# Optimization experiments

Hardware: AMD Instinct MI355X
Metric: run time of the kernel (lower is better)

The kernel has to match this reference:

```python
import jax, jax.numpy as jnp
import numpy as np

N = 100000
E = 3200000
HID = 256
C = 10
T = 12
D = 8
HEADS = 4
LH = HID // 2  # LSTM hidden = hidden_dim // 2


def setup_inputs() -> dict:
    key = jax.random.key(0)
    ks = jax.random.split(key, 16)
    rn = lambda k, shp, s=0.05: jax.random.normal(k, shp, dtype=jnp.float32) * s
    return {
        "embeddings": jax.random.normal(ks[0], (N, HID), dtype=jnp.float32),
        "predictions": jax.random.normal(ks[1], (N, C), dtype=jnp.float32),
        "temporal_features": jax.random.normal(ks[2], (N, T, D), dtype=jnp.float32),
        "edge_index": jax.random.randint(ks[3], (2, E), 0, N),
        "cW1": rn(ks[4], (HID // 2, HID)), "cb1": jnp.zeros((HID // 2,), jnp.float32),
        "cW2": rn(ks[5], (1, HID // 2)), "cb2": jnp.zeros((1,), jnp.float32),
        "w_ih0": rn(ks[6], (4 * LH, C)), "w_hh0": rn(ks[7], (4 * LH, LH)),
        "b_ih0": jnp.zeros((4 * LH,), jnp.float32), "b_hh0": jnp.zeros((4 * LH,), jnp.float32),
        "w_ih1": rn(ks[8], (4 * LH, LH)), "w_hh1": rn(ks[9], (4 * LH, LH)),
        "b_ih1": jnp.zeros((4 * LH,), jnp.float32), "b_hh1": jnp.zeros((4 * LH,), jnp.float32),
        "gW": rn(ks[10], (C, HEADS * C)), "ga_src": rn(ks[11], (HEADS, C)),
        "ga_dst": rn(ks[12], (HEADS, C)), "gb": jnp.zeros((C,), jnp.float32),
    }


def _lstm_layer(x, w_ih, w_hh, b_ih, b_hh):
    # x: [N, T, I]; PyTorch gate order i, f, g, o
    n = x.shape[0]
    h_dim = w_hh.shape[1]
    def step(carry, xt):
        h, c = carry
        g = xt @ w_ih.T + h @ w_hh.T + b_ih + b_hh  # [N, 4H]
        i, f, gg, o = jnp.split(g, 4, axis=-1)
        c = jax.nn.sigmoid(f) * c + jax.nn.sigmoid(i) * jnp.tanh(gg)
        h = jax.nn.sigmoid(o) * jnp.tanh(c)
        return (h, c), h
    init = (jnp.zeros((n, h_dim), x.dtype), jnp.zeros((n, h_dim), x.dtype))
    _, hs = jax.lax.scan(step, init, jnp.swapaxes(x, 0, 1))  # [T, N, H]
    return jnp.swapaxes(hs, 0, 1)


def _gat(probs, src, dst, gW, ga_src, ga_dst, gb, n):
    x = (probs @ gW).reshape(n, HEADS, C)  # [N, H, C]
    a_s = (x * ga_src).sum(-1)  # [N, H]
    a_d = (x * ga_dst).sum(-1)
    e = jax.nn.leaky_relu(a_s[src] + a_d[dst], 0.2)  # [E, H]
    m = jax.ops.segment_max(e, dst, num_segments=n)
    ex = jnp.exp(e - m[dst])
    s = jax.ops.segment_sum(ex, dst, num_segments=n)
    alpha = ex / (s[dst] + 1e-16)  # edge softmax per destination
    out = jax.ops.segment_sum(alpha[:, :, None] * x[src], dst, num_segments=n)
    return out.mean(axis=1) + gb  # concat=False -> head mean, plus bias


def reference(embeddings, predictions, temporal_features, edge_index,
              cW1, cb1, cW2, cb2,
              w_ih0, w_hh0, b_ih0, b_hh0, w_ih1, w_hh1, b_ih1, b_hh1,
              gW, ga_src, ga_dst, gb):
    n = predictions.shape[0]
    probs = jax.nn.softmax(predictions, axis=-1)
    max_probs = probs.max(axis=-1)
    pseudo_labels = jnp.argmax(probs, axis=-1)

    # confidence_net (dropout inactive in eval)
    h = jax.nn.relu(embeddings @ cW1.T + cb1)
    embedding_confidence = jax.nn.sigmoid(h @ cW2.T + cb2)[:, 0]

    # temporal consistency: same prediction repeated T times through 2-layer LSTM
    t = temporal_features.shape[1]
    pred_seq = jnp.broadcast_to(predictions[:, None, :], (n, t, predictions.shape[1]))
    l1 = _lstm_layer(pred_seq, w_ih0, w_hh0, b_ih0, b_hh0)
    l2 = _lstm_layer(l1, w_ih1, w_hh1, b_ih1, b_hh1)
    temporal_variance = jnp.var(l2, axis=1, ddof=1).mean(axis=-1)  # torch.var unbiased
    temporal_confidence = 1.0 / (1.0 + temporal_variance)

    # self-loops (used by both GATConv and agreement check)
    loops = jnp.arange(n, dtype=edge_index.dtype)
    src = jnp.concatenate([edge_index[0], loops])
    dst = jnp.concatenate([edge_index[1], loops])

    gout = _gat(probs, src, dst, gW, ga_src, ga_dst, gb, n)
    num = (probs * gout).sum(-1)
    den = jnp.maximum(jnp.linalg.norm(probs, axis=-1) * jnp.linalg.norm(gout, axis=-1), 1e-8)
    graph_confidence = ((num / den) + 1.0) / 2.0

    combined = (0.4 * max_probs + 0.2 * embedding_confidence
                + 0.2 * temporal_confidence + 0.2 * graph_confidence)
    confident_mask = combined > 0.85

    # neighborhood agreement via segment-sum scatter (replaces per-edge loop)
    deg = jax.ops.segment_sum(jnp.ones_like(src, jnp.float32), src, num_segments=n)
    oh = jax.nn.one_hot(pseudo_labels, C, dtype=jnp.float32)
    nsum = jax.ops.segment_sum(oh[src], dst, num_segments=n)
    navg = nsum / (deg[:, None] + 1e-8)
    agreement = jnp.take_along_axis(navg, pseudo_labels[:, None], axis=1)[:, 0] >= 0.6
    final_mask = confident_mask & agreement

    entropy = -(probs * jnp.log(probs + 1e-8)).sum(-1)
    uncertainty = entropy / np.log(C).astype(np.float32)

    return (pseudo_labels, combined, final_mask, max_probs,
            embedding_confidence, temporal_confidence, graph_confidence, uncertainty)
```

## Files before the change

kernel.cpp:

```cpp
#include <hip/hip_runtime.h>
#include <hip/hip_bf16.h>


#define HIDN 256
#define NC 10
#define TSTEPS 12
#define NHEADS 4
#define LH 128

typedef __attribute__((ext_vector_type(8))) short short8;
typedef __attribute__((ext_vector_type(4))) float floatx4;

__device__ __forceinline__ unsigned short f2bf(float x) {
  unsigned u = __float_as_uint(x);
  u = u + 0x7FFFu + ((u >> 16) & 1u);
  return (unsigned short)(u >> 16);
}
__device__ __forceinline__ unsigned char f2fp8(float x) {
  return (unsigned char)(__builtin_amdgcn_cvt_pk_fp8_f32(x, 0.f, 0, false) & 0xff);
}
__device__ __forceinline__ float fexp2(float x) { return __builtin_amdgcn_exp2f(x); }
__device__ __forceinline__ float frcpf(float x) { return __builtin_amdgcn_rcpf(x); }
#define LOG2E 1.44269504f
__device__ __forceinline__ float sigf(float x) {
  return frcpf(1.0f + fexp2(-LOG2E * x));
}
__device__ __forceinline__ float sig2(float x) {
  return frcpf(1.f + fexp2(-LOG2E * x));
}
__device__ __forceinline__ float tanh2(float x) {
  return 1.f - 2.f * frcpf(1.f + fexp2((2.f * LOG2E) * x));
}
__device__ __forceinline__ floatx4 mfma16(short8 a, short8 b, floatx4 c) {
  return __builtin_amdgcn_mfma_f32_16x16x32_bf16(a, b, c, 0, 0, 0);
}
__device__ __forceinline__ floatx4 mfma8(long a, long b, floatx4 c) {
  return __builtin_amdgcn_mfma_f32_16x16x32_fp8_fp8(a, b, c, 0, 0, 0);
}

__global__ __launch_bounds__(256) void probs_kernel(
    const float* __restrict__ pred, const float* __restrict__ gW,
    const float* __restrict__ gas, const float* __restrict__ gad,
    float* __restrict__ out, float* __restrict__ wp12,
    float* __restrict__ was, float* __restrict__ wad,
    int* __restrict__ wlab, float* __restrict__ wmp, int N) {
  __shared__ float sgW[400], sgas[40], sgad[40];
  int tid = threadIdx.x;
  for (int i = tid; i < 400; i += 256) sgW[i] = gW[i];
  if (tid < 40) { sgas[tid] = gas[tid]; sgad[tid] = gad[tid]; }
  __syncthreads();
  int node = blockIdx.x * 256 + tid;
  if (node >= N) return;
  const float* pr = pred + (size_t)node * NC;
  float p[NC];
#pragma unroll
  for (int c = 0; c < NC; c++) p[c] = pr[c];
  float pm = p[0]; int arg = 0;
#pragma unroll
  for (int c = 1; c < NC; c++) if (p[c] > pm) { pm = p[c]; arg = c; }
  float s = 0.f, prb[NC];
#pragma unroll
  for (int c = 0; c < NC; c++) { prb[c] = __expf(p[c] - pm); s += prb[c]; }
  float inv = 1.f / s;
  float ent = 0.f;
#pragma unroll
  for (int c = 0; c < NC; c++) {
    prb[c] *= inv;
    ent -= prb[c] * __logf(prb[c] + 1e-8f);
  }
  float4* wp = (float4*)(wp12 + (size_t)node * 12);
  wp[0] = make_float4(prb[0], prb[1], prb[2], prb[3]);
  wp[1] = make_float4(prb[4], prb[5], prb[6], prb[7]);
  wp[2] = make_float4(prb[8], prb[9], 0.f, 0.f);
  out[node] = (float)arg;
  out[(size_t)3 * N + node] = inv;
  out[(size_t)7 * N + node] = ent * (1.f / 2.302585093f);
  wlab[node] = arg;
  wmp[node] = inv;
  float xv[40];
#pragma unroll
  for (int hc = 0; hc < 40; hc++) {
    float t = 0.f;
#pragma unroll
    for (int k = 0; k < NC; k++) t += prb[k] * sgW[k * 40 + hc];
    xv[hc] = t;
  }
#pragma unroll
  for (int h = 0; h < NHEADS; h++) {
    float as = 0.f, ad = 0.f;
#pragma unroll
    for (int c = 0; c < NC; c++) { as += xv[h * 10 + c] * sgas[h * 10 + c]; ad += xv[h * 10 + c] * sgad[h * 10 + c]; }
    was[(size_t)node * 4 + h] = as;
    wad[(size_t)node * 4 + h] = ad;
  }
}

__global__ __launch_bounds__(256) void pack_kernel(
    const float* __restrict__ whh0, const float* __restrict__ wih0,
    const float* __restrict__ wih1, const float* __restrict__ whh1,
    const float* __restrict__ cw1,
    unsigned char* __restrict__ PB1, unsigned char* __restrict__ PB2,
    unsigned short* __restrict__ PBc) {
  int idx = blockIdx.x * 256 + threadIdx.x;
  if (idx < 81920) {
    int j = idx & 7, lane = (idx >> 3) & 63, rest = idx >> 9;
    int g = rest & 3, w = (rest >> 2) & 7, ks = rest >> 5;
    int k = ks * 32 + ((lane >> 4) << 3) + j;
    int u = w * 16 + (lane & 15), row = g * 128 + u;
    float val = 0.f;
    if (k < 128) val = whh0[row * 128 + k];
    else if (k < 138) val = wih0[row * 10 + (k - 128)];
    PB1[idx] = f2fp8(val);
  }
  if (idx < 131072) {
    int j = idx & 7, lane = (idx >> 3) & 63, rest = idx >> 9;
    int g = rest & 3, w = (rest >> 2) & 7, ks = rest >> 5;
    int k = ks * 32 + ((lane >> 4) << 3) + j;
    int u = w * 16 + (lane & 15), row = g * 128 + u;
    float val = (k < 128) ? wih1[row * 128 + k] : whh1[row * 128 + (k - 128)];
    PB2[idx] = f2fp8(val);
  }
  if (idx < 32768) {
    int j = idx & 7, lane = (idx >> 3) & 63, t2 = idx >> 9;
    int ti = t2 & 7, ks = t2 >> 3;
    int n = ti * 16 + (lane & 15);
    int k = ks * 32 + ((lane >> 4) << 3) + j;
    PBc[idx] = f2bf(cw1[n * 256 + k]);
  }
}

__global__ void rankhist_kernel(const int* __restrict__ ei, int* __restrict__ indeg,
                                int* __restrict__ outdeg, int* __restrict__ erank,
                                int E, int N) {
  int idx = blockIdx.x * 256 + threadIdx.x;
  if (idx >= E + N) return;
  int src, dst;
  if (idx < E) { src = ei[idx]; dst = ei[E + idx]; } else { src = dst = idx - E; }
  int r = atomicAdd(&indeg[dst], 1);
  atomicAdd(&outdeg[src], 1);
  erank[idx] = r;
}

__device__ __forceinline__ void conf_body(
    int bb, unsigned short* astage,
    const float* __restrict__ emb, const unsigned short* __restrict__ PBc,
    const float* __restrict__ cb1, const float* __restrict__ cw2,
    const float* __restrict__ cb2, float* __restrict__ wec, int N) {
  int tid = threadIdx.x;
  int base = bb * 128;
  for (int i = tid * 4; i < 128 * 256; i += 1024) {
    int row = i >> 8, col = i & 255;
    float4 v = make_float4(0.f, 0.f, 0.f, 0.f);
    if (base + row < N) v = *(const float4*)(emb + (size_t)(base + row) * 256 + col);
    unsigned short* d = &astage[row * 264 + col];
    d[0] = f2bf(v.x); d[1] = f2bf(v.y); d[2] = f2bf(v.z); d[3] = f2bf(v.w);
  }
  __syncthreads();
  int wave = tid >> 6, lane = tid & 63, quad = lane >> 4, ln = lane & 15;
  float b1f[8], w2f[8];
#pragma unroll
  for (int t = 0; t < 8; t++) { b1f[t] = cb1[t * 16 + ln]; w2f[t] = cw2[t * 16 + ln]; }
  floatx4 acc[2][8];
#pragma unroll
  for (int mi = 0; mi < 2; mi++)
#pragma unroll
    for (int t = 0; t < 8; t++) acc[mi][t] = (floatx4){b1f[t], b1f[t], b1f[t], b1f[t]};
#pragma unroll
  for (int ks = 0; ks < 8; ks++) {
    short8 a0 = *(const short8*)&astage[(wave * 32 + ln) * 264 + ks * 32 + quad * 8];
    short8 a1 = *(const short8*)&astage[(wave * 32 + 16 + ln) * 264 + ks * 32 + quad * 8];
    const unsigned short* bp = PBc + (((size_t)(ks * 8) * 64 + lane) << 3);
#pragma unroll
    for (int t = 0; t < 8; t++) {
      short8 b = *(const short8*)(bp + (size_t)t * 512);
      acc[0][t] = mfma16(a0, b, acc[0][t]);
      acc[1][t] = mfma16(a1, b, acc[1][t]);
    }
  }
  float part[2][4];
#pragma unroll
  for (int mi = 0; mi < 2; mi++)
#pragma unroll
    for (int r = 0; r < 4; r++) {
      float t = 0.f;
#pragma unroll
      for (int ti = 0; ti < 8; ti++) t += fmaxf(acc[mi][ti][r], 0.f) * w2f[ti];
      part[mi][r] = t;
    }
#pragma unroll
  for (int off = 8; off >= 1; off >>= 1)
#pragma unroll
    for (int mi = 0; mi < 2; mi++)
#pragma unroll
      for (int r = 0; r < 4; r++) part[mi][r] += __shfl_xor(part[mi][r], off);
  if (ln == 0) {
    float b2 = cb2[0];
#pragma unroll
    for (int mi = 0; mi < 2; mi++)
#pragma unroll
      for (int r = 0; r < 4; r++) {
        int node = base + wave * 32 + mi * 16 + quad * 4 + r;
        if (node < N) wec[node] = sigf(part[mi][r] + b2);
      }
  }
}

__device__ __forceinline__ void scan_body(
    int* wsum, const int* __restrict__ indeg, int* __restrict__ rowptr, int N) {
  int t = threadIdx.x;
  int lane = t & 63, wv = t >> 6;
  int runbase = 0;
  for (int c0 = 0; c0 < N; c0 += 1024) {
    int i = c0 + t * 4;
    int v0 = 0, v1 = 0, v2 = 0, v3 = 0;
    if (i + 0 < N) v0 = indeg[i + 0];
    if (i + 1 < N) v1 = indeg[i + 1];
    if (i + 2 < N) v2 = indeg[i + 2];
    if (i + 3 < N) v3 = indeg[i + 3];
    int tsum = v0 + v1 + v2 + v3;
    int x = tsum;
#pragma unroll
    for (int d = 1; d < 64; d <<= 1) { int y = __shfl_up(x, d); if (lane >= d) x += y; }
    if (lane == 63) wsum[wv] = x;
    __syncthreads();
    int wo = 0;
    for (int w = 0; w < wv; w++) wo += wsum[w];
    int tot = wsum[0] + wsum[1] + wsum[2] + wsum[3];
    int excl = runbase + wo + x - tsum;
    if (i + 0 < N) rowptr[i + 0] = excl;
    if (i + 1 < N) rowptr[i + 1] = excl + v0;
    if (i + 2 < N) rowptr[i + 2] = excl + v0 + v1;
    if (i + 3 < N) rowptr[i + 3] = excl + v0 + v1 + v2;
    runbase += tot;
    __syncthreads();
  }
  if (t == 0) rowptr[N] = runbase;
}

__global__ __launch_bounds__(256) void mega2_kernel(
    const float* __restrict__ emb, const unsigned short* __restrict__ PBc,
    const float* __restrict__ cb1, const float* __restrict__ cw2,
    const float* __restrict__ cb2, float* __restrict__ wec,
    const int* __restrict__ indeg, int* __restrict__ rowptr, int N, int GC) {
  __shared__ __align__(16) unsigned short astage[128 * 264];
  int b = blockIdx.x;
  if (b < GC) {
    conf_body(b, astage, emb, PBc, cb1, cw2, cb2, wec, N);
  } else {
    scan_body((int*)astage, indeg, rowptr, N);
  }
}

__global__ void scatterrank_kernel(const int* __restrict__ ei,
                                   const int* __restrict__ rowptr,
                                   const int* __restrict__ erank,
                                   int* __restrict__ csr, int E, int N) {
  int idx = blockIdx.x * 256 + threadIdx.x;
  if (idx >= E + N) return;
  int src, dst;
  if (idx < E) { src = ei[idx]; dst = ei[E + idx]; } else { src = dst = idx - E; }
  csr[rowptr[dst] + erank[idx]] = src;
}

__global__ __launch_bounds__(256) void gather_kernel(
    const int* __restrict__ rowptr, const int* __restrict__ csr,
    const float* __restrict__ was, const float* __restrict__ wad,
    const float* __restrict__ wp12, const int* __restrict__ wlab,
    const int* __restrict__ outdeg, const float* __restrict__ gW,
    const float* __restrict__ gb, float* __restrict__ wgc,
    float* __restrict__ wag, int N) {
  __shared__ float sgW[400];
  int tid = threadIdx.x;
  for (int i = tid; i < 400; i += 256) sgW[i] = gW[i];
  __syncthreads();
  int vgid = blockIdx.x * 256 + tid;
  int node = vgid >> 4, sub = vgid & 15, h = sub & 3, par = sub >> 2;
  if (node >= N) return;
  int beg = rowptr[node], end = rowptr[node + 1];
  float ad = wad[(size_t)node * 4 + h];
  int mylab = wlab[node];
  float ssum = 0.f, cnt = 0.f;
  float z[10];
#pragma unroll
  for (int c = 0; c < 10; c++) z[c] = 0.f;
  for (int e = beg + par; e < end; e += 4) {
    int s = csr[e];
    float v = was[(size_t)s * 4 + h] + ad;
    float lr = v >= 0.f ? v : 0.2f * v;
    float ex = fexp2(LOG2E * lr);
    ssum += ex;
    const float4* pp = (const float4*)(wp12 + (size_t)s * 12);
    float4 p0 = pp[0], p1 = pp[1], p2 = pp[2];
    z[0] += ex * p0.x; z[1] += ex * p0.y; z[2] += ex * p0.z; z[3] += ex * p0.w;
    z[4] += ex * p1.x; z[5] += ex * p1.y; z[6] += ex * p1.z; z[7] += ex * p1.w;
    z[8] += ex * p2.x; z[9] += ex * p2.y;
    cnt += (wlab[s] == mylab) ? 1.f : 0.f;
  }
  ssum += __shfl_xor(ssum, 4); ssum += __shfl_xor(ssum, 8);
  cnt  += __shfl_xor(cnt, 4);  cnt  += __shfl_xor(cnt, 8);
#pragma unroll
  for (int c = 0; c < 10; c++) { z[c] += __shfl_xor(z[c], 4); z[c] += __shfl_xor(z[c], 8); }
  float inv = 1.f / (ssum + 1e-16f);
  float gpart[10];
#pragma unroll
  for (int c = 0; c < 10; c++) {
    float t = 0.f;
#pragma unroll
    for (int k = 0; k < 10; k++) t += z[k] * sgW[k * 40 + h * 10 + c];
    gpart[c] = t * inv;
  }
#pragma unroll
  for (int c = 0; c < 10; c++) {
    gpart[c] += __shfl_xor(gpart[c], 1);
    gpart[c] += __shfl_xor(gpart[c], 2);
  }
  if (sub == 0) {
    float num = 0.f, np2 = 0.f, ng2 = 0.f;
    const float* pn = wp12 + (size_t)node * 12;
#pragma unroll
    for (int c = 0; c < 10; c++) {
      float g = gpart[c] * 0.25f + gb[c];
      float p = pn[c];
      num += p * g;
      np2 += p * p;
      ng2 += g * g;
    }
    float den = fmaxf(sqrtf(np2) * sqrtf(ng2), 1e-8f);
    wgc[node] = (num / den + 1.f) * 0.5f;
    float dgv = (float)outdeg[node];
    wag[node] = cnt / (dgv + 1e-8f);
  }
}

#define HB2 4352

__global__ __launch_bounds__(512, 2) void lstm_kernel(
    const float* __restrict__ pred, const unsigned char* __restrict__ PB1,
    const unsigned char* __restrict__ PB2,
    const float* __restrict__ bih0, const float* __restrict__ bhh0,
    const float* __restrict__ bih1, const float* __restrict__ bhh1,
    const float* __restrict__ wmp, const float* __restrict__ wec,
    const float* __restrict__ wgc, const float* __restrict__ wag,
    float* __restrict__ out, int N) {
  __shared__ __align__(16) unsigned char hb[4 * HB2];
  __shared__ __align__(16) unsigned char xbuf[32 * 40];
  __shared__ float varsum[32];
  int tid = threadIdx.x;
  int base = blockIdx.x * 32;
  for (int i = tid * 4; i < HB2; i += 2048) *(int*)&hb[3 * HB2 + i] = 0;
  for (int i = tid; i < 32 * 40; i += 512) {
    int nd = i / 40, o = i - nd * 40;
    float v = 0.f;
    if (o < 10 && base + nd < N) v = pred[(size_t)(base + nd) * NC + o];
    xbuf[i] = f2fp8(v);
  }
  if (tid < 32) varsum[tid] = 0.f;
  int wave = tid >> 6, lane = tid & 63, quad = lane >> 4, ln = lane & 15;
  float b0f[4], b1f[4];
#pragma unroll
  for (int g = 0; g < 4; g++) {
    int row = g * 128 + wave * 16 + ln;
    b0f[g] = bih0[row] + bhh0[row];
    b1f[g] = bih1[row] + bhh1[row];
  }
  long w1r[5][4], w2r[8][4];
#pragma unroll
  for (int ks = 0; ks < 5; ks++)
#pragma unroll
    for (int g = 0; g < 4; g++)
      w1r[ks][g] = *(const long*)(PB1 + (size_t)(((ks * 8 + wave) * 4 + g) * 64 + lane) * 8);
#pragma unroll
  for (int ks = 0; ks < 8; ks++)
#pragma unroll
    for (int g = 0; g < 4; g++)
      w2r[ks][g] = *(const long*)(PB2 + (size_t)(((ks * 8 + wave) * 4 + g) * 64 + lane) * 8);
  float c1[8], c2[8], s1[8], s2[8];
#pragma unroll
  for (int i = 0; i < 8; i++) { c1[i] = 0.f; c2[i] = 0.f; s1[i] = 0.f; s2[i] = 0.f; }
  const int hq = quad * 8;
  const int ucol = wave * 16 + ln;
  int arow[2], wrow[2];
#pragma unroll
  for (int mt = 0; mt < 2; mt++) {
    arow[mt] = (mt * 16 + ln) * 136 + hq;
    wrow[mt] = (mt * 16 + quad * 4) * 136 + ucol;
  }
  __syncthreads();
  long xa[2];
  xa[0] = *(const long*)&xbuf[ln * 40 + hq];
  xa[1] = *(const long*)&xbuf[(16 + ln) * 40 + hq];

  {
    floatx4 acc[2][4];
#pragma unroll
    for (int mt = 0; mt < 2; mt++)
#pragma unroll
      for (int g = 0; g < 4; g++) acc[mt][g] = (floatx4){b0f[g], b0f[g], b0f[g], b0f[g]};
#pragma unroll
    for (int g = 0; g < 4; g++)
#pragma unroll
      for (int mt = 0; mt < 2; mt++) acc[mt][g] = mfma8(xa[mt], w1r[4][g], acc[mt][g]);
#pragma unroll
    for (int mt = 0; mt < 2; mt++)
#pragma unroll
      for (int r = 0; r < 4; r++) {
        int ci = mt * 4 + r;
        float ig = sig2(acc[mt][0][r]);
        float gg = tanh2(acc[mt][2][r]);
        float og = sig2(acc[mt][3][r]);
        float c = ig * gg;
        c1[ci] = c;
        hb[0 + wrow[mt] + r * 136] = f2fp8(og * tanh2(c));
      }
  }

#define LSTM_SEG(O1R, O1W, O2R, O2W, lastseg)                                    \
  {                                                                              \
    __syncthreads();                                                             \
    floatx4 acc[2][4];                                                           \
    _Pragma("unroll") for (int mt = 0; mt < 2; mt++)                             \
        _Pragma("unroll") for (int g = 0; g < 4; g++)                            \
            acc[mt][g] = (floatx4){b1f[g], b1f[g], b1f[g], b1f[g]};              \
    _Pragma("unroll") for (int ks = 0; ks < 8; ks++) {                           \
      long a_[2];                                                                \
      if (ks < 4) {                                                              \
        _Pragma("unroll") for (int mt = 0; mt < 2; mt++)                         \
            a_[mt] = *(const long*)&hb[(O1R) + arow[mt] + ks * 32];              \
      } else {                                                                   \
        _Pragma("unroll") for (int mt = 0; mt < 2; mt++)                         \
            a_[mt] = *(const long*)&hb[(O2R) + arow[mt] + (ks - 4) * 32];        \
      }                                                                          \
      _Pragma("unroll") for (int g = 0; g < 4; g++)                              \
          _Pragma("unroll") for (int mt = 0; mt < 2; mt++)                       \
              acc[mt][g] = mfma8(a_[mt], w2r[ks][g], acc[mt][g]);                \
    }                                                                            \
    _Pragma("unroll") for (int mt = 0; mt < 2; mt++)                             \
        _Pragma("unroll") for (int r = 0; r < 4; r++) {                          \
      int ci = mt * 4 + r;                                                       \
      float ig = sig2(acc[mt][0][r]);                                            \
      float fg = sig2(acc[mt][1][r]);                                            \
      float gg = tanh2(acc[mt][2][r]);                                           \
      float og = sig2(acc[mt][3][r]);                                            \
      float c = fg * c2[ci] + ig * gg;                                           \
      c2[ci] = c;                                                                \
      float h = og * tanh2(c);                                                   \
      s1[ci] += h;                                                               \
      s2[ci] += h * h;                                                           \
      hb[(O2W) + wrow[mt] + r * 136] = f2fp8(h);                                 \
    }                                                                            \
    if (!(lastseg)) {                                                            \
      _Pragma("unroll") for (int mt = 0; mt < 2; mt++)                           \
          _Pragma("unroll") for (int g = 0; g < 4; g++)                          \
              acc[mt][g] = (floatx4){b0f[g], b0f[g], b0f[g], b0f[g]};            \
      _Pragma("unroll") for (int ks = 0; ks < 5; ks++) {                         \
        long a_[2];                                                              \
        if (ks < 4) {                                                            \
          _Pragma("unroll") for (int mt = 0; mt < 2; mt++)                       \
              a_[mt] = *(const long*)&hb[(O1R) + arow[mt] + ks * 32];            \
        } else {                                                                 \
          a_[0] = xa[0]; a_[1] = xa[1];                                          \
        }                                                                        \
        _Pragma("unroll") for (int g = 0; g < 4; g++)                            \
            _Pragma("unroll") for (int mt = 0; mt < 2; mt++)                     \
                acc[mt][g] = mfma8(a_[mt], w1r[ks][g], acc[mt][g]);              \
      }                                                                          \
      _Pragma("unroll") for (int mt = 0; mt < 2; mt++)                           \
          _Pragma("unroll") for (int r = 0; r < 4; r++) {                        \
        int ci = mt * 4 + r;                                                     \
        float ig = sig2(acc[mt][0][r]);                                          \
        float fg = sig2(acc[mt][1][r]);                                          \
        float gg = tanh2(acc[mt][2][r]);                                         \
        float og = sig2(acc[mt][3][r]);                                          \
        float c = fg * c1[ci] + ig * gg;                                         \
        c1[ci] = c;                                                              \
        hb[(O1W) + wrow[mt] + r * 136] = f2fp8(og * tanh2(c));                   \
      }                                                                          \
    }                                                                            \
  }

  for (int tt = 0; tt < TSTEPS / 2; tt++) {
    LSTM_SEG(0, HB2, 3 * HB2, 2 * HB2, false);
    LSTM_SEG(HB2, 0, 2 * HB2, 3 * HB2, tt == TSTEPS / 2 - 1);
  }
#undef LSTM_SEG

#pragma unroll
  for (int mt = 0; mt < 2; mt++)
#pragma unroll
    for (int r = 0; r < 4; r++) {
      int ci = mt * 4 + r;
      float m = s1[ci] * (1.f / 12.f);
      float var = (s2[ci] - 12.f * m * m) * (1.f / 11.f);
      atomicAdd(&varsum[mt * 16 + quad * 4 + r], var);
    }
  __syncthreads();
  if (tid < 32 && base + tid < N) {
    int node = base + tid;
    float tc = 1.f / (1.f + varsum[tid] * (1.f / 128.f));
    float mp = wmp[node], ec = wec[node], gc = wgc[node];
    float comb = 0.4f * mp + 0.2f * ec + 0.2f * tc + 0.2f * gc;
    bool mask = (comb > 0.85f) && (wag[node] >= 0.6f);
    out[(size_t)1 * N + node] = comb;
    out[(size_t)2 * N + node] = mask ? 1.f : 0.f;
    out[(size_t)4 * N + node] = ec;
    out[(size_t)5 * N + node] = tc;
    out[(size_t)6 * N + node] = gc;
  }
}

extern "C" void kernel_launch(void* const* d_in, const int* in_sizes, int n_in,
                              void* d_out, int out_size, void* d_ws, size_t ws_size,
                              hipStream_t stream) {
  const float* emb  = (const float*)d_in[0];
  const float* pred = (const float*)d_in[1];
  const int*   ei   = (const int*)d_in[3];
  const float* cw1  = (const float*)d_in[4];
  const float* cb1  = (const float*)d_in[5];
  const float* cw2  = (const float*)d_in[6];
  const float* cb2  = (const float*)d_in[7];
  const float* wih0 = (const float*)d_in[8];
  const float* whh0 = (const float*)d_in[9];
  const float* bih0 = (const float*)d_in[10];
  const float* bhh0 = (const float*)d_in[11];
  const float* wih1 = (const float*)d_in[12];
  const float* whh1 = (const float*)d_in[13];
  const float* bih1 = (const float*)d_in[14];
  const float* bhh1 = (const float*)d_in[15];
  const float* gW   = (const float*)d_in[16];
  const float* gas  = (const float*)d_in[17];
  const float* gad  = (const float*)d_in[18];
  const float* gb   = (const float*)d_in[19];

  const int N = in_sizes[0] / HIDN;
  const int E = in_sizes[3] / 2;
  float* out = (float*)d_out;
  float* ws = (float*)d_ws;
  const size_t sN = (size_t)N;
  const size_t sE = (size_t)E;

  float* wp12   = ws;
  float* was    = ws + 12 * sN;
  float* wad    = ws + 16 * sN;
  int*   wlab   = (int*)(ws + 20 * sN);
  float* wmp    = ws + 21 * sN;
  float* wec    = ws + 22 * sN;
  float* wgc    = ws + 24 * sN;
  float* wag    = ws + 25 * sN;
  int* indeg    = (int*)(ws + 26 * sN);
  int* outdeg   = (int*)(ws + 27 * sN);
  int* rowptr   = (int*)(ws + 28 * sN);
  int* erank    = (int*)(ws + 29 * sN) + 64;
  int* csr      = erank + sE + sN + 64;
  float* pbase  = (float*)(csr + sE + sN + 64);
  unsigned char* PB1 = (unsigned char*)pbase;
  unsigned char* PB2 = (unsigned char*)(pbase + 20480);
  unsigned short* PBc = (unsigned short*)(pbase + 53248);

  hipMemsetAsync(indeg, 0, 2 * sN * sizeof(int), stream);

  probs_kernel<<<(N + 255) / 256, 256, 0, stream>>>(
      pred, gW, gas, gad, out, wp12, was, wad, wlab, wmp, N);
  pack_kernel<<<512, 256, 0, stream>>>(whh0, wih0, wih1, whh1, cw1, PB1, PB2, PBc);
  int ne = E + N;
  rankhist_kernel<<<(ne + 255) / 256, 256, 0, stream>>>(ei, indeg, outdeg, erank, E, N);

  int GC = (N + 127) / 128;
  mega2_kernel<<<GC + 1, 256, 0, stream>>>(
      emb, PBc, cb1, cw2, cb2, wec, indeg, rowptr, N, GC);

  scatterrank_kernel<<<(ne + 255) / 256, 256, 0, stream>>>(ei, rowptr, erank, csr, E, N);

  gather_kernel<<<(16 * N + 255) / 256, 256, 0, stream>>>(
      rowptr, csr, was, wad, wp12, wlab, outdeg, gW, gb, wgc, wag, N);

  lstm_kernel<<<(N + 31) / 32, 512, 0, stream>>>(
      pred, PB1, PB2, bih0, bhh0, bih1, bhh1, wmp, wec, wgc, wag, out, N);
}
```

Before: 1.412 ms.

## Shard degree atomics, parallelize CSR scan, pack node records, and restructure GAT gather

Degree counting now goes into 8 sharded histograms keyed by block, which is meant to reduce atomic contention on hot nodes. The single-block serial prefix scan is replaced by a three-kernel parallel scan that also computes per-shard bases. Probabilities, source attention scores and the label are packed into one 64-byte record per node, so each edge needs a single contiguous fetch. The gather kernel uses 4 threads per node that process all heads per edge instead of 16 threads each handling one head, which cuts redundant neighbor loads but raises register use and adds extra kernel launches and memset traffic.

```diff
diff --git a/kernel.cpp b/kernel.cpp
--- a/kernel.cpp
+++ b/kernel.cpp
@@ -41,9 +41,8 @@
 __global__ __launch_bounds__(256) void probs_kernel(
     const float* __restrict__ pred, const float* __restrict__ gW,
     const float* __restrict__ gas, const float* __restrict__ gad,
-    float* __restrict__ out, float* __restrict__ wp12,
-    float* __restrict__ was, float* __restrict__ wad,
-    int* __restrict__ wlab, float* __restrict__ wmp, int N) {
+    float* __restrict__ out, float* __restrict__ wp16,
+    float* __restrict__ wad, float* __restrict__ wmp, int N) {
   __shared__ float sgW[400], sgas[40], sgad[40];
   int tid = threadIdx.x;
   for (int i = tid; i < 400; i += 256) sgW[i] = gW[i];
@@ -68,14 +67,9 @@
     prb[c] *= inv;
     ent -= prb[c] * __logf(prb[c] + 1e-8f);
   }
-  float4* wp = (float4*)(wp12 + (size_t)node * 12);
-  wp[0] = make_float4(prb[0], prb[1], prb[2], prb[3]);
-  wp[1] = make_float4(prb[4], prb[5], prb[6], prb[7]);
-  wp[2] = make_float4(prb[8], prb[9], 0.f, 0.f);
   out[node] = (float)arg;
   out[(size_t)3 * N + node] = inv;
   out[(size_t)7 * N + node] = ent * (1.f / 2.302585093f);
-  wlab[node] = arg;
   wmp[node] = inv;
   float xv[40];
 #pragma unroll
@@ -85,14 +79,20 @@
     for (int k = 0; k < NC; k++) t += prb[k] * sgW[k * 40 + hc];
     xv[hc] = t;
   }
+  float asv[4];
 #pragma unroll
   for (int h = 0; h < NHEADS; h++) {
     float as = 0.f, ad = 0.f;
 #pragma unroll
     for (int c = 0; c < NC; c++) { as += xv[h * 10 + c] * sgas[h * 10 + c]; ad += xv[h * 10 + c] * sgad[h * 10 + c]; }
-    was[(size_t)node * 4 + h] = as;
+    asv[h] = as;
     wad[(size_t)node * 4 + h] = ad;
   }
+  float4* wp = (float4*)(wp16 + (size_t)node * 16);
+  wp[0] = make_float4(prb[0], prb[1], prb[2], prb[3]);
+  wp[1] = make_float4(prb[4], prb[5], prb[6], prb[7]);
+  wp[2] = make_float4(prb[8], prb[9], asv[0], asv[1]);
+  wp[3] = make_float4(asv[2], asv[3], __int_as_float(arg), 0.f);
 }
 
 __global__ __launch_bounds__(256) void pack_kernel(
@@ -129,25 +129,26 @@
   }
 }
 
-__global__ void rankhist_kernel(const int* __restrict__ ei, int* __restrict__ indeg,
-                                int* __restrict__ outdeg, int* __restrict__ erank,
+__global__ void rankhist_kernel(const int* __restrict__ ei, int* __restrict__ shin,
+                                int* __restrict__ shout, int* __restrict__ erank,
                                 int E, int N) {
   int idx = blockIdx.x * 256 + threadIdx.x;
   if (idx >= E + N) return;
+  int sh = blockIdx.x & 7;
   int src, dst;
   if (idx < E) { src = ei[idx]; dst = ei[E + idx]; } else { src = dst = idx - E; }
-  int r = atomicAdd(&indeg[dst], 1);
-  atomicAdd(&outdeg[src], 1);
+  int r = atomicAdd(&shin[(size_t)sh * N + dst], 1);
+  atomicAdd(&shout[(size_t)sh * N + src], 1);
   erank[idx] = r;
 }
 
-__device__ __forceinline__ void conf_body(
-    int bb, unsigned short* astage,
+__global__ __launch_bounds__(256) void conf_kernel(
     const float* __restrict__ emb, const unsigned short* __restrict__ PBc,
     const float* __restrict__ cb1, const float* __restrict__ cw2,
     const float* __restrict__ cb2, float* __restrict__ wec, int N) {
+  __shared__ __align__(16) unsigned short astage[128 * 264];
   int tid = threadIdx.x;
-  int base = bb * 128;
+  int base = blockIdx.x * 128;
   for (int i = tid * 4; i < 128 * 256; i += 1024) {
     int row = i >> 8, col = i & 255;
     float4 v = make_float4(0.f, 0.f, 0.f, 0.f);
@@ -205,67 +206,90 @@
   }
 }
 
-__device__ __forceinline__ void scan_body(
-    int* wsum, const int* __restrict__ indeg, int* __restrict__ rowptr, int N) {
+__global__ __launch_bounds__(256) void scan1_kernel(
+    const int* __restrict__ shin, const int* __restrict__ shout,
+    int* __restrict__ shbase, int* __restrict__ outdeg,
+    int* __restrict__ rowptr, int* __restrict__ partials, int N) {
+  int t = threadIdx.x, b = blockIdx.x;
+  int base = b * 1024 + t * 4;
+  int tot[4];
+#pragma unroll
+  for (int j = 0; j < 4; j++) {
+    int i = base + j;
+    int run = 0;
+    if (i < N) {
+      int od = 0;
+#pragma unroll
+      for (int sh = 0; sh < 8; sh++) {
+        int v = shin[(size_t)sh * N + i];
+        shbase[(size_t)sh * N + i] = run;
+        run += v;
+        od += shout[(size_t)sh * N + i];
+      }
+      outdeg[i] = od;
+    }
+    tot[j] = run;
+  }
+  int tsum = tot[0] + tot[1] + tot[2] + tot[3];
+  int lane = t & 63, wv = t >> 6;
+  int x = tsum;
+#pragma unroll
+  for (int d = 1; d < 64; d <<= 1) { int y = __shfl_up(x, d); if (lane >= d) x += y; }
+  __shared__ int wsum[4];
+  if (lane == 63) wsum[wv] = x;
+  __syncthreads();
+  int wo = 0;
+  for (int i = 0; i < wv; i++) wo += wsum[i];
+  int excl = wo + x - tsum;
+  if (base + 0 < N) rowptr[base + 0] = excl;
+  if (base + 1 < N) rowptr[base + 1] = excl + tot[0];
+  if (base + 2 < N) rowptr[base + 2] = excl + tot[0] + tot[1];
+  if (base + 3 < N) rowptr[base + 3] = excl + tot[0] + tot[1] + tot[2];
+  if (t == 255) partials[b] = wo + x;
+}
+
+__global__ void scan2_kernel(int* __restrict__ partials, int nb) {
   int t = threadIdx.x;
   int lane = t & 63, wv = t >> 6;
-  int runbase = 0;
-  for (int c0 = 0; c0 < N; c0 += 1024) {
-    int i = c0 + t * 4;
-    int v0 = 0, v1 = 0, v2 = 0, v3 = 0;
-    if (i + 0 < N) v0 = indeg[i + 0];
-    if (i + 1 < N) v1 = indeg[i + 1];
-    if (i + 2 < N) v2 = indeg[i + 2];
-    if (i + 3 < N) v3 = indeg[i + 3];
-    int tsum = v0 + v1 + v2 + v3;
-    int x = tsum;
-#pragma unroll
-    for (int d = 1; d < 64; d <<= 1) { int y = __shfl_up(x, d); if (lane >= d) x += y; }
-    if (lane == 63) wsum[wv] = x;
-    __syncthreads();
-    int wo = 0;
-    for (int w = 0; w < wv; w++) wo += wsum[w];
-    int tot = wsum[0] + wsum[1] + wsum[2] + wsum[3];
-    int excl = runbase + wo + x - tsum;
-    if (i + 0 < N) rowptr[i + 0] = excl;
-    if (i + 1 < N) rowptr[i + 1] = excl + v0;
-    if (i + 2 < N) rowptr[i + 2] = excl + v0 + v1;
-    if (i + 3 < N) rowptr[i + 3] = excl + v0 + v1 + v2;
-    runbase += tot;
-    __syncthreads();
-  }
-  if (t == 0) rowptr[N] = runbase;
-}
-
-__global__ __launch_bounds__(256) void mega2_kernel(
-    const float* __restrict__ emb, const unsigned short* __restrict__ PBc,
-    const float* __restrict__ cb1, const float* __restrict__ cw2,
-    const float* __restrict__ cb2, float* __restrict__ wec,
-    const int* __restrict__ indeg, int* __restrict__ rowptr, int N, int GC) {
-  __shared__ __align__(16) unsigned short astage[128 * 264];
-  int b = blockIdx.x;
-  if (b < GC) {
-    conf_body(b, astage, emb, PBc, cb1, cw2, cb2, wec, N);
-  } else {
-    scan_body((int*)astage, indeg, rowptr, N);
-  }
+  int v = (t < nb) ? partials[t] : 0;
+  int x = v;
+#pragma unroll
+  for (int d = 1; d < 64; d <<= 1) { int y = __shfl_up(x, d); if (lane >= d) x += y; }
+  __shared__ int wsum[4];
+  if (lane == 63) wsum[wv] = x;
+  __syncthreads();
+  int wo = 0;
+  for (int i = 0; i < wv; i++) wo += wsum[i];
+  if (t < nb) partials[t] = wo + x - v;
+}
+
+__global__ void scan3_kernel(int* __restrict__ rowptr, int* __restrict__ shbase,
+                             const int* __restrict__ partials, int N, int total) {
+  int i = blockIdx.x * 256 + threadIdx.x;
+  if (i < N) {
+    int r = rowptr[i] + partials[i >> 10];
+    rowptr[i] = r;
+#pragma unroll
+    for (int sh = 0; sh < 8; sh++) shbase[(size_t)sh * N + i] += r;
+  }
+  if (i == 0) rowptr[N] = total;
 }
 
 __global__ void scatterrank_kernel(const int* __restrict__ ei,
-                                   const int* __restrict__ rowptr,
+                                   const int* __restrict__ shbase,
                                    const int* __restrict__ erank,
                                    int* __restrict__ csr, int E, int N) {
   int idx = blockIdx.x * 256 + threadIdx.x;
   if (idx >= E + N) return;
+  int sh = (idx >> 8) & 7;
   int src, dst;
   if (idx < E) { src = ei[idx]; dst = ei[E + idx]; } else { src = dst = idx - E; }
-  csr[rowptr[dst] + erank[idx]] = src;
+  csr[shbase[(size_t)sh * N + dst] + erank[idx]] = src;
 }
 
 __global__ __launch_bounds__(256) void gather_kernel(
     const int* __restrict__ rowptr, const int* __restrict__ csr,
-    const float* __restrict__ was, const float* __restrict__ wad,
-    const float* __restrict__ wp12, const int* __restrict__ wlab,
+    const float* __restrict__ wp16, const float* __restrict__ wad,
     const int* __restrict__ outdeg, const float* __restrict__ gW,
     const float* __restrict__ gb, float* __restrict__ wgc,
     float* __restrict__ wag, int N) {
@@ -274,39 +298,69 @@
   for (int i = tid; i < 400; i += 256) sgW[i] = gW[i];
   __syncthreads();
   int vgid = blockIdx.x * 256 + tid;
-  int node = vgid >> 4, sub = vgid & 15, h = sub & 3, par = sub >> 2;
+  int node = vgid >> 2, par = vgid & 3;
   if (node >= N) return;
   int beg = rowptr[node], end = rowptr[node + 1];
-  float ad = wad[(size_t)node * 4 + h];
-  int mylab = wlab[node];
-  float ssum = 0.f, cnt = 0.f;
-  float z[10];
-#pragma unroll
-  for (int c = 0; c < 10; c++) z[c] = 0.f;
+  float4 ad4 = *(const float4*)(wad + (size_t)node * 4);
+  const float4* myrec = (const float4*)(wp16 + (size_t)node * 16);
+  float4 m3 = myrec[3];
+  int mylab = __float_as_int(m3.z);
+  float ssum0 = 0.f, ssum1 = 0.f, ssum2 = 0.f, ssum3 = 0.f, cnt = 0.f;
+  float z[4][10];
+#pragma unroll
+  for (int h = 0; h < 4; h++)
+#pragma unroll
+    for (int c = 0; c < 10; c++) z[h][c] = 0.f;
   for (int e = beg + par; e < end; e += 4) {
     int s = csr[e];
-    float v = was[(size_t)s * 4 + h] + ad;
-    float lr = v >= 0.f ? v : 0.2f * v;
-    float ex = fexp2(LOG2E * lr);
-    ssum += ex;
-    const float4* pp = (const float4*)(wp12 + (size_t)s * 12);
-    float4 p0 = pp[0], p1 = pp[1], p2 = pp[2];
-    z[0] += ex * p0.x; z[1] += ex * p0.y; z[2] += ex * p0.z; z[3] += ex * p0.w;
-    z[4] += ex * p1.x; z[5] += ex * p1.y; z[6] += ex * p1.z; z[7] += ex * p1.w;
-    z[8] += ex * p2.x; z[9] += ex * p2.y;
-    cnt += (wlab[s] == mylab) ? 1.f : 0.f;
-  }
-  ssum += __shfl_xor(ssum, 4); ssum += __shfl_xor(ssum, 8);
-  cnt  += __shfl_xor(cnt, 4);  cnt  += __shfl_xor(cnt, 8);
-#pragma unroll
-  for (int c = 0; c < 10; c++) { z[c] += __shfl_xor(z[c], 4); z[c] += __shfl_xor(z[c], 8); }
-  float inv = 1.f / (ssum + 1e-16f);
+    const float4* rp = (const float4*)(wp16 + (size_t)s * 16);
+    float4 r0 = rp[0], r1 = rp[1], r2 = rp[2], r3 = rp[3];
+    float p[10] = {r0.x, r0.y, r0.z, r0.w, r1.x, r1.y, r1.z, r1.w, r2.x, r2.y};
+    float as[4] = {r2.z, r2.w, r3.x, r3.y};
+    float adh[4] = {ad4.x, ad4.y, ad4.z, ad4.w};
+    cnt += (__float_as_int(r3.z) == mylab) ? 1.f : 0.f;
+#pragma unroll
+    for (int h = 0; h < 4; h++) {
+      float v = as[h] + adh[h];
+      float lr = v >= 0.f ? v : 0.2f * v;
+      float ex = fexp2(LOG2E * lr);
+      if (h == 0) ssum0 += ex; else if (h == 1) ssum1 += ex;
+      else if (h == 2) ssum2 += ex; else ssum3 += ex;
+#pragma unroll
+      for (int c = 0; c < 10; c++) z[h][c] += ex * p[c];
+    }
+  }
+#pragma unroll
+  for (int mask = 1; mask <= 2; mask <<= 1) {
+    cnt += __shfl_xor(cnt, mask);
+    ssum0 += __shfl_xor(ssum0, mask); ssum1 += __shfl_xor(ssum1, mask);
+    ssum2 += __shfl_xor(ssum2, mask); ssum3 += __shfl_xor(ssum3, mask);
+#pragma unroll
+    for (int h = 0; h < 4; h++)
+#pragma unroll
+      for (int c = 0; c < 10; c++) z[h][c] += __shfl_xor(z[h][c], mask);
+  }
+  float zp[10], sp;
+  if (par == 0) { sp = ssum0;
+#pragma unroll
+    for (int c = 0; c < 10; c++) zp[c] = z[0][c];
+  } else if (par == 1) { sp = ssum1;
+#pragma unroll
+    for (int c = 0; c < 10; c++) zp[c] = z[1][c];
+  } else if (par == 2) { sp = ssum2;
+#pragma unroll
+    for (int c = 0; c < 10; c++) zp[c] = z[2][c];
+  } else { sp = ssum3;
+#pragma unroll
+    for (int c = 0; c < 10; c++) zp[c] = z[3][c];
+  }
+  float inv = 1.f / (sp + 1e-16f);
   float gpart[10];
 #pragma unroll
   for (int c = 0; c < 10; c++) {
     float t = 0.f;
 #pragma unroll
-    for (int k = 0; k < 10; k++) t += z[k] * sgW[k * 40 + h * 10 + c];
+    for (int k = 0; k < 10; k++) t += zp[k] * sgW[k * 40 + par * 10 + c];
     gpart[c] = t * inv;
   }
 #pragma unroll
@@ -314,9 +368,10 @@
     gpart[c] += __shfl_xor(gpart[c], 1);
     gpart[c] += __shfl_xor(gpart[c], 2);
   }
-  if (sub == 0) {
+  if (par == 0) {
+    float4 m0 = myrec[0], m1 = myrec[1], m2 = myrec[2];
+    float pn[10] = {m0.x, m0.y, m0.z, m0.w, m1.x, m1.y, m1.z, m1.w, m2.x, m2.y};
     float num = 0.f, np2 = 0.f, ng2 = 0.f;
-    const float* pn = wp12 + (size_t)node * 12;
 #pragma unroll
     for (int c = 0; c < 10; c++) {
       float g = gpart[c] * 0.25f + gb[c];
@@ -538,40 +593,44 @@
   const size_t sN = (size_t)N;
   const size_t sE = (size_t)E;
 
-  float* wp12   = ws;
-  float* was    = ws + 12 * sN;
+  float* wp16   = ws;
   float* wad    = ws + 16 * sN;
-  int*   wlab   = (int*)(ws + 20 * sN);
-  float* wmp    = ws + 21 * sN;
-  float* wec    = ws + 22 * sN;
-  float* wgc    = ws + 24 * sN;
-  float* wag    = ws + 25 * sN;
-  int* indeg    = (int*)(ws + 26 * sN);
-  int* outdeg   = (int*)(ws + 27 * sN);
-  int* rowptr   = (int*)(ws + 28 * sN);
-  int* erank    = (int*)(ws + 29 * sN) + 64;
+  float* wmp    = ws + 20 * sN;
+  float* wec    = ws + 21 * sN;
+  float* wgc    = ws + 22 * sN;
+  float* wag    = ws + 23 * sN;
+  int* outdeg   = (int*)(ws + 24 * sN);
+  int* rowptr   = (int*)(ws + 25 * sN);
+  int* shin     = (int*)(ws + 26 * sN) + 64;
+  int* shout    = shin + 8 * sN;
+  int* shbase   = shout + 8 * sN;
+  int* partials = shbase + 8 * sN + 64;
+  int* erank    = partials + 256 + 64;
   int* csr      = erank + sE + sN + 64;
   float* pbase  = (float*)(csr + sE + sN + 64);
   unsigned char* PB1 = (unsigned char*)pbase;
   unsigned char* PB2 = (unsigned char*)(pbase + 20480);
   unsigned short* PBc = (unsigned short*)(pbase + 53248);
 
-  hipMemsetAsync(indeg, 0, 2 * sN * sizeof(int), stream);
+  hipMemsetAsync(shin, 0, 16 * sN * sizeof(int), stream);
 
   probs_kernel<<<(N + 255) / 256, 256, 0, stream>>>(
-      pred, gW, gas, gad, out, wp12, was, wad, wlab, wmp, N);
+      pred, gW, gas, gad, out, wp16, wad, wmp, N);
   pack_kernel<<<512, 256, 0, stream>>>(whh0, wih0, wih1, whh1, cw1, PB1, PB2, PBc);
   int ne = E + N;
-  rankhist_kernel<<<(ne + 255) / 256, 256, 0, stream>>>(ei, indeg, outdeg, erank, E, N);
-
-  int GC = (N + 127) / 128;
-  mega2_kernel<<<GC + 1, 256, 0, stream>>>(
-      emb, PBc, cb1, cw2, cb2, wec, indeg, rowptr, N, GC);
-
-  scatterrank_kernel<<<(ne + 255) / 256, 256, 0, stream>>>(ei, rowptr, erank, csr, E, N);
-
-  gather_kernel<<<(16 * N + 255) / 256, 256, 0, stream>>>(
-      rowptr, csr, was, wad, wp12, wlab, outdeg, gW, gb, wgc, wag, N);
+  rankhist_kernel<<<(ne + 255) / 256, 256, 0, stream>>>(ei, shin, shout, erank, E, N);
+
+  conf_kernel<<<(N + 127) / 128, 256, 0, stream>>>(emb, PBc, cb1, cw2, cb2, wec, N);
+
+  int nb = (N + 1023) / 1024;
+  scan1_kernel<<<nb, 256, 0, stream>>>(shin, shout, shbase, outdeg, rowptr, partials, N);
+  scan2_kernel<<<1, 256, 0, stream>>>(partials, nb);
+  scan3_kernel<<<(N + 255) / 256, 256, 0, stream>>>(rowptr, shbase, partials, N, ne);
+
+  scatterrank_kernel<<<(ne + 255) / 256, 256, 0, stream>>>(ei, shbase, erank, csr, E, N);
+
+  gather_kernel<<<(4 * N + 255) / 256, 256, 0, stream>>>(
+      rowptr, csr, wp16, wad, outdeg, gW, gb, wgc, wag, N);
 
   lstm_kernel<<<(N + 31) / 32, 512, 0, stream>>>(
       pred, PB1, PB2, bih0, bhh0, bih1, bhh1, wmp, wec, wgc, wag, out, N);
```

After: 1.332 ms. -5.6%, faster.
